# Kernel optimization log

Measured on AMD Instinct MI355X. Metric: run time of the kernel, lower is better.

Reference implementation:

```python
import jax, jax.numpy as jnp
import numpy as np

N_STACK = 32
ZERO_OFFSET = 1e-6
EPS = 1e-8
POW_EPS = 1e-12  # guard for 0**sharpen gradient


def _cos_sim(a, b):
    # a: [D] param, b: [B, D]; matches torch.cosine_similarity with eps=1e-8
    an = jnp.maximum(jnp.sqrt(jnp.sum(a * a)), EPS)
    bn = jnp.maximum(jnp.sqrt(jnp.sum(b * b, axis=-1)), EPS)
    return (b @ a) / (an * bn)


def _elu(x):
    return jnp.where(x > 0, x, jnp.expm1(x))


def setup_inputs() -> dict:
    key = jax.random.key(0)
    k0, k1, k2, k3 = jax.random.split(key, 4)
    B, T, D = 128, 256, 256
    return {
        "x": jax.random.normal(k0, (B, T, D), jnp.float32),
        "should_pop": jax.random.normal(k1, (D,), jnp.float32),
        "sharpen_pointer": jnp.array([5.0], jnp.float32),
        "latch_enable": jax.random.normal(k2, (D,), jnp.float32) * 0.01,
        "latch_init": jax.random.normal(k3, (B, D), jnp.float32),
    }


def _forward(x, should_pop, sharpen_pointer, latch_enable, latch_init):
    B, T, D = x.shape
    dtype = x.dtype
    stack0 = jnp.full((B, N_STACK, D), ZERO_OFFSET, dtype)
    ptr0 = jnp.full((B, N_STACK), ZERO_OFFSET, dtype).at[:, 0].set(1.0)
    sharpen = sharpen_pointer[0]

    def step(carry, inp):
        stack, ptr, latch = carry  # [B,N,D], [B,N], [B,D]
        # pop gate from PREVIOUS latch state (relay of length 1)
        pop = _elu(_cos_sim(should_pop, latch))            # [B]
        push = 1.0 - pop
        # push branch: advance pointer, write value at new slot
        p_push = jnp.roll(ptr, 1, axis=1)
        st_push = stack * (1.0 - p_push)[..., None] + inp[:, None, :] * p_push[..., None]
        # pop branch: erase current slot to zero_offset, retreat pointer
        st_pop = stack * (1.0 - ptr)[..., None] + ZERO_OFFSET * ptr[..., None]
        p_pop = jnp.roll(ptr, -1, axis=1)
        # superpose push/pop (null_op weight is exactly 0 in this module)
        new_stack = push[:, None, None] * st_push + pop[:, None, None] * st_pop
        new_ptr = push[:, None] * p_push + pop[:, None] * p_pop
        # sharpen pointer: relu, pow, renormalize
        p = jnp.maximum(jax.nn.relu(new_ptr), POW_EPS) ** sharpen
        p = p / jnp.maximum(jnp.sum(p, axis=1, keepdims=True), EPS)
        # read and gate output
        s = jnp.einsum('bnv,bn->bv', new_stack, p)
        out = pop[:, None] * s
        # latch update: gate = elu(cos(enable_param, inp)); dropout is eval-mode no-op
        g = _elu(_cos_sim(latch_enable, inp))
        new_latch = g[:, None] * inp + (1.0 - g)[:, None] * latch
        return (new_stack, p, new_latch), out

    _, outs = jax.lax.scan(step, (stack0, ptr0, latch_init), jnp.swapaxes(x, 0, 1))
    return jnp.swapaxes(outs, 0, 1)  # [B, T, D]


def reference(x, should_pop, sharpen_pointer, latch_enable, latch_init):
    return _forward(x, should_pop, sharpen_pointer, latch_enable, latch_init)
```

## Files before the change

kernel.cpp:

```cpp
#include <hip/hip_runtime.h>
#include <math.h>


#define NSTK 32
#define DDIM 256
#define ZO 1e-6f
#define EPSC 1e-8f
#define PEPS 1e-12f
#define TTILE 32
#define MAXT 1024
#define CH 4

__device__ __forceinline__ float elu_f(float c) {
    return (c > 0.f) ? c : expm1f(c);
}

__device__ __forceinline__ float dpp_xor1(float x) {
    return __int_as_float(__builtin_amdgcn_update_dpp(0, __float_as_int(x), 0xB1, 0xF, 0xF, true));
}
__device__ __forceinline__ float dpp_xor2(float x) {
    return __int_as_float(__builtin_amdgcn_update_dpp(0, __float_as_int(x), 0x4E, 0xF, 0xF, true));
}
__device__ __forceinline__ float dpp_halfmirror(float x) {
    return __int_as_float(__builtin_amdgcn_update_dpp(0, __float_as_int(x), 0x141, 0xF, 0xF, true));
}
__device__ __forceinline__ float dpp_mirror(float x) {
    return __int_as_float(__builtin_amdgcn_update_dpp(0, __float_as_int(x), 0x140, 0xF, 0xF, true));
}
__device__ __forceinline__ float swz_xor16(float x) {
    return __int_as_float(__builtin_amdgcn_ds_swizzle(__float_as_int(x), 0x401F));
}

__device__ __forceinline__ float xor16_sum(float x) {
    float a = x, b = x;
    asm("v_permlane16_swap_b32 %0, %1" : "+v"(a), "+v"(b));
    return a + b;
}
__device__ __forceinline__ float xor32_sum(float x) {
    float a = x, b = x;
    asm("v_permlane32_swap_b32 %0, %1" : "+v"(a), "+v"(b));
    return a + b;
}

__global__ void gate4_kernel(const float* __restrict__ vecs,
                             const float* __restrict__ par,
                             float* __restrict__ gout,
                             int T) {
    const int b = blockIdx.y;
    const int t = blockIdx.x * 4 + (threadIdx.x >> 6);
    const int lane = threadIdx.x & 63;
    const float4 v = *(const float4*)(vecs + ((size_t)b * T + t) * DDIM + lane * 4);
    const float4 p = *(const float4*)(par + lane * 4);
    float r0 = v.x * p.x + v.y * p.y + v.z * p.z + v.w * p.w;
    float r1 = v.x * v.x + v.y * v.y + v.z * v.z + v.w * v.w;
    float r2 = p.x * p.x + p.y * p.y + p.z * p.z + p.w * p.w;
#pragma unroll
    for (int off = 32; off >= 1; off >>= 1) {
        r0 += __shfl_xor(r0, off, 64);
        r1 += __shfl_xor(r1, off, 64);
        r2 += __shfl_xor(r2, off, 64);
    }
    if (lane == 0) {
        const float c = r0 / (fmaxf(sqrtf(r2), EPSC) * fmaxf(sqrtf(r1), EPSC));
        gout[(size_t)b * T + t] = elu_f(c);
    }
}

__global__ void latch_scan_kernel(const float* __restrict__ x,
                                  const float* __restrict__ latch0,
                                  const float* __restrict__ g,
                                  float* __restrict__ L,
                                  int T) {
    const int b = blockIdx.x >> 2;
    const int dt = blockIdx.x & 3;
    const int d = dt * 64 + threadIdx.x;
    const float* xb = x + (size_t)b * T * DDIM + d;
    const float* gb = g + (size_t)b * T;
    float* Lb = L + (size_t)b * T * DDIM + d;
    float l = latch0[(size_t)b * DDIM + d];
    for (int c = 0; c < T; c += 32) {
        float xv[32], gv[32];
#pragma unroll
        for (int i = 0; i < 32; i++) xv[i] = xb[(size_t)(c + i) * DDIM];
#pragma unroll
        for (int i = 0; i < 32; i++) gv[i] = gb[c + i];
#pragma unroll
        for (int i = 0; i < 32; i++) {
            Lb[(size_t)(c + i) * DDIM] = l;
            l = fmaf(gv[i], xv[i] - l, l);
        }
    }
}

__launch_bounds__(64, 1)
__global__ void ptr_scan_kernel(const float* __restrict__ pop_arr,
                                const float* __restrict__ sharpen_ptr,
                                float* __restrict__ Parr,
                                int T) {
    const int b0 = blockIdx.x * 2;
    const int tid = threadIdx.x;
    const int n = tid & 31;
    const int grp = tid >> 5;
    const float sharpen = sharpen_ptr[0];
    const bool sharp5 = (sharpen == 5.0f);

    __shared__ float pops[2 * MAXT];
    for (int i = tid; i < 2 * T; i += 64) pops[i] = pop_arr[(size_t)b0 * T + i];
    __syncthreads();
    const float* popg = pops + grp * T;
    float* Pb = Parr + (size_t)(b0 + grp) * T * 32;

    float u = (n == 0) ? 1.0f : ZO;
    float invu = 1.0f;
    int t = 0;

    auto step = [&](float pop) {
        const float push = 1.0f - pop;
        const float up = __shfl(u, (n + 31) & 31, 32);
        const float un = __shfl(u, (n + 1) & 31, 32);
        const float r = fmaf(push, up, pop * un);
        const float q = fmaxf(r * invu, PEPS);
        float unew;
        if (sharp5) { const float q2 = q * q, q4 = q2 * q2; unew = q4 * q; }
        else        { unew = exp2f(sharpen * log2f(q)); }
        float s = unew;
        s += dpp_xor1(s);
        s += dpp_xor2(s);
        s += dpp_halfmirror(s);
        s += dpp_mirror(s);
        s += swz_xor16(s);
        const float invn = 1.0f / fmaxf(s, EPSC);
        Pb[(size_t)t * 32 + n] = unew * invn;
        u = unew; invu = invn;
        t++;
    };

    const float4* p4 = (const float4*)popg;
    float4 cA0 = p4[0], cA1 = p4[1], cA2 = p4[2], cA3 = p4[3];
    for (int c = 0; c < T; c += 16) {
        float4 cB0, cB1, cB2, cB3;
        if (c + 16 < T) {
            const float4* pn4 = p4 + (c + 16) / 4;
            cB0 = pn4[0]; cB1 = pn4[1]; cB2 = pn4[2]; cB3 = pn4[3];
        }
        step(cA0.x); step(cA0.y); step(cA0.z); step(cA0.w);
        step(cA1.x); step(cA1.y); step(cA1.z); step(cA1.w);
        step(cA2.x); step(cA2.y); step(cA2.z); step(cA2.w);
        step(cA3.x); step(cA3.y); step(cA3.z); step(cA3.w);
        if (c + 16 < T) { cA0 = cB0; cA1 = cB1; cA2 = cB2; cA3 = cB3; }
    }
}

#define LOADC(PN, XN, PMN, POPN, t0) do {                                    \
    _Pragma("unroll") for (int i = 0; i < CH; i++) {                         \
        PN[i][0] = *(const float4*)(Pb + (size_t)((t0) + i) * 32);           \
        PN[i][1] = *(const float4*)(Pb + (size_t)((t0) + i) * 32 + 4);       \
        XN[i] = xb[(size_t)((t0) + i) * DDIM];                               \
        PMN[i] = Pm1b[(size_t)((t0) + i) * 32];                              \
        POPN[i] = popb[(t0) + i];                                            \
    } } while (0)

#define STEPS(PN, XN, PMN, POPN, tg) do {                                    \
    _Pragma("unroll") for (int i = 0; i < CH; i++) {                         \
        const float pop = POPN[i];                                           \
        const float push = 1.0f - pop;                                       \
        const float xv = XN[i];                                              \
        const float pn[8] = {PN[i][0].x, PN[i][0].y, PN[i][0].z, PN[i][0].w, \
                             PN[i][1].x, PN[i][1].y, PN[i][1].z, PN[i][1].w};\
        float acc = 0.f;                                                     \
        _Pragma("unroll") for (int j = 0; j < 8; j++) {                      \
            const float p_s = pc[j];                                         \
            const float pp_s = (j == 0) ? pm1 : pc[j - 1];                   \
            const float t0v = pop * p_s;                                     \
            const float m = fmaf(push, pp_s, t0v);                           \
            const float alpha = 1.0f - m;                                    \
            const float beta = push * pp_s;                                  \
            const float bxg = fmaf(beta, xv, ZO * t0v);                      \
            const float ns = fmaf(alpha, st[j], bxg);                        \
            st[j] = ns;                                                      \
            acc = fmaf(pn[j], ns, acc);                                      \
        }                                                                    \
        _Pragma("unroll") for (int j = 0; j < 8; j++) pc[j] = pn[j];         \
        pm1 = PMN[i];                                                        \
        acc = xor16_sum(acc);                                                \
        acc = xor32_sum(acc);                                                \
        if (lane < 16) ob[(size_t)((tg) + i) * DDIM] = pop * acc;            \
    } } while (0)

__launch_bounds__(64, 1)
__global__ void stack_kernel(const float* __restrict__ x,
                             const float* __restrict__ Parr,
                             const float* __restrict__ pop_arr,
                             float* __restrict__ out,
                             int T) {
    const int b = blockIdx.y;
    const int dtile = blockIdx.x;
    const int lane = threadIdx.x;
    const int dsub = lane & 15;
    const int ng = lane >> 4;

    const float* Pb = Parr + (size_t)b * T * 32 + ng * 8;
    const int pm1_idx = (ng * 8 + 31) & 31;
    const float* Pm1b = Parr + (size_t)b * T * 32 + pm1_idx;
    const float* xb = x + (size_t)b * T * DDIM + dtile * 16 + dsub;
    const float* popb = pop_arr + (size_t)b * T;
    float* ob = out + (size_t)b * T * DDIM + dtile * 16 + dsub;

    float st[8], pc[8];
#pragma unroll
    for (int j = 0; j < 8; j++) { st[j] = ZO; pc[j] = ZO; }
    if (ng == 0) pc[0] = 1.0f;
    float pm1 = ZO;

    float4 PA[CH][2], PB[CH][2];
    float xA[CH], xB[CH], pmA[CH], pmB[CH], popA[CH], popB[CH];

    LOADC(PA, xA, pmA, popA, 0);
    for (int c = 0; c < T; c += 2 * CH) {
        if (c + CH < T) LOADC(PB, xB, pmB, popB, c + CH);
        STEPS(PA, xA, pmA, popA, c);
        if (c + 2 * CH < T) LOADC(PA, xA, pmA, popA, c + 2 * CH);
        STEPS(PB, xB, pmB, popB, c + CH);
    }
}

__launch_bounds__(256, 1)
__global__ void neuralstack_kernel(const float* __restrict__ x,
                                   const float* __restrict__ should_pop,
                                   const float* __restrict__ sharpen_ptr,
                                   const float* __restrict__ latch_enable,
                                   const float* __restrict__ latch_init,
                                   float* __restrict__ out,
                                   int T) {
    const int b = blockIdx.x;
    const int tid = threadIdx.x;
    const int wave = tid >> 6;
    const int lane = tid & 63;
    __shared__ float red[2][16];
    const float sp_d = should_pop[tid];
    const float le_d = latch_enable[tid];
    const float sharpen = sharpen_ptr[0];
    float latch = latch_init[(size_t)b * DDIM + tid];
    float a0 = sp_d * sp_d, a1 = le_d * le_d;
#pragma unroll
    for (int off = 32; off >= 1; off >>= 1) {
        a0 += __shfl_xor(a0, off, 64);
        a1 += __shfl_xor(a1, off, 64);
    }
    if (lane == 0) { red[0][wave * 4] = a0; red[0][wave * 4 + 1] = a1; }
    __syncthreads();
    const float an_sp = fmaxf(sqrtf(red[0][0] + red[0][4] + red[0][8] + red[0][12]), EPSC);
    const float an_le = fmaxf(sqrtf(red[0][1] + red[0][5] + red[0][9] + red[0][13]), EPSC);
    __syncthreads();
    float st[NSTK], ptr[NSTK];
#pragma unroll
    for (int n = 0; n < NSTK; n++) { st[n] = ZO; ptr[n] = (n == 0) ? 1.0f : ZO; }
    const float* xb = x + (size_t)b * T * DDIM + tid;
    float* ob = out + (size_t)b * T * DDIM + tid;
    const bool sharp5 = (sharpen == 5.0f);
    float inp = xb[0];
    for (int t = 0; t < T; t++) {
        const int tn = (t + 1 < T) ? (t + 1) : (T - 1);
        const float inp_next = xb[(size_t)tn * DDIM];
        float r0 = sp_d * latch, r1 = latch * latch, r2 = le_d * inp, r3 = inp * inp;
#pragma unroll
        for (int off = 32; off >= 1; off >>= 1) {
            r0 += __shfl_xor(r0, off, 64);
            r1 += __shfl_xor(r1, off, 64);
            r2 += __shfl_xor(r2, off, 64);
            r3 += __shfl_xor(r3, off, 64);
        }
        const int buf = t & 1;
        if (lane == 0) {
            red[buf][wave * 4] = r0; red[buf][wave * 4 + 1] = r1;
            red[buf][wave * 4 + 2] = r2; red[buf][wave * 4 + 3] = r3;
        }
        __syncthreads();
        const float s0 = red[buf][0] + red[buf][4] + red[buf][8] + red[buf][12];
        const float s1 = red[buf][1] + red[buf][5] + red[buf][9] + red[buf][13];
        const float s2 = red[buf][2] + red[buf][6] + red[buf][10] + red[buf][14];
        const float s3 = red[buf][3] + red[buf][7] + red[buf][11] + red[buf][15];
        const float pop = elu_f(s0 / (an_sp * fmaxf(sqrtf(s1), EPSC)));
        const float push = 1.0f - pop;
        const float g = elu_f(s2 / (an_le * fmaxf(sqrtf(s3), EPSC)));
        float q[NSTK];
#pragma unroll
        for (int n = 0; n < NSTK; n++) {
            const float pp = ptr[(n + NSTK - 1) & (NSTK - 1)];
            const float pn = ptr[(n + 1) & (NSTK - 1)];
            q[n] = fmaxf(push * pp + pop * pn, PEPS);
        }
        if (sharp5) {
#pragma unroll
            for (int n = 0; n < NSTK; n++) { const float v = q[n], v2 = v * v; q[n] = v2 * v2 * v; }
        } else {
#pragma unroll
            for (int n = 0; n < NSTK; n++) q[n] = exp2f(sharpen * log2f(q[n]));
        }
        float qa = 0.f, qb = 0.f, qc = 0.f, qd = 0.f;
#pragma unroll
        for (int n = 0; n < NSTK; n += 4) { qa += q[n]; qb += q[n+1]; qc += q[n+2]; qd += q[n+3]; }
        const float inv = 1.0f / fmaxf((qa + qb) + (qc + qd), EPSC);
        float sacc = 0.f;
#pragma unroll
        for (int n = 0; n < NSTK; n++) {
            const float pp = ptr[(n + NSTK - 1) & (NSTK - 1)];
            const float pc_ = ptr[n];
            const float ns = push * (st[n] + pp * (inp - st[n])) + pop * (st[n] + pc_ * (ZO - st[n]));
            st[n] = ns;
            sacc += ns * (q[n] * inv);
        }
#pragma unroll
        for (int n = 0; n < NSTK; n++) ptr[n] = q[n] * inv;
        ob[(size_t)t * DDIM] = pop * sacc;
        latch = fmaf(g, inp - latch, latch);
        inp = inp_next;
    }
}

extern "C" void kernel_launch(void* const* d_in, const int* in_sizes, int n_in,
                              void* d_out, int out_size, void* d_ws, size_t ws_size,
                              hipStream_t stream) {
    const float* x = (const float*)d_in[0];
    const float* should_pop = (const float*)d_in[1];
    const float* sharpen_ptr = (const float*)d_in[2];
    const float* latch_enable = (const float*)d_in[3];
    const float* latch_init = (const float*)d_in[4];
    float* out = (float*)d_out;

    const int D = in_sizes[1];
    const int B = in_sizes[4] / D;
    const int T = in_sizes[0] / in_sizes[4];
    (void)n_in; (void)out_size;

    const size_t BT = (size_t)B * T;
    const size_t off_g = 0;
    const size_t off_pop = BT;
    const size_t off_L = 2 * BT;
    const size_t off_P = off_L + BT * D;
    const size_t need_floats = off_P + BT * 32;

    if (ws_size < need_floats * sizeof(float) || D != DDIM ||
        (T % TTILE) != 0 || (B % 2) != 0 || T > MAXT) {
        neuralstack_kernel<<<B, 256, 0, stream>>>(x, should_pop, sharpen_ptr,
                                                  latch_enable, latch_init, out, T);
        return;
    }

    float* ws = (float*)d_ws;
    float* g = ws + off_g;
    float* pop = ws + off_pop;
    float* L = ws + off_L;
    float* P = ws + off_P;

    gate4_kernel<<<dim3(T / 4, B), 256, 0, stream>>>(x, latch_enable, g, T);
    latch_scan_kernel<<<B * 4, 64, 0, stream>>>(x, latch_init, g, L, T);
    gate4_kernel<<<dim3(T / 4, B), 256, 0, stream>>>(L, should_pop, pop, T);
    ptr_scan_kernel<<<B / 2, 64, 0, stream>>>(pop, sharpen_ptr, P, T);
    stack_kernel<<<dim3(D / 16, B), 64, 0, stream>>>(x, P, pop, out, T);
}
```

Baseline: 237.2 us.

## Precompute per-step stack coefficients in a separate kernel before the stack scan

Adds a coef_kernel that computes, for every batch, step and stack slot, the alpha/beta/zero-offset/read-weight coefficients from the pointer and pop arrays. It stores them as float4 in the workspace region that previously held the latch buffer. The stack scan then only does two FMAs plus the accumulate per slot, and no longer tracks the previous pointer in registers. The trade is an extra kernel launch and about 4x more coefficient traffic per step, read redundantly by all 16 d-tiles. The prefetch depth also drops from 4-step chunks to a single step ahead.

```diff
diff --git a/kernel.cpp b/kernel.cpp
--- a/kernel.cpp
+++ b/kernel.cpp
@@ -7,9 +7,7 @@
 #define ZO 1e-6f
 #define EPSC 1e-8f
 #define PEPS 1e-12f
-#define TTILE 32
 #define MAXT 1024
-#define CH 4
 
 __device__ __forceinline__ float elu_f(float c) {
     return (c > 0.f) ? c : expm1f(c);
@@ -151,45 +149,60 @@
     }
 }
 
-#define LOADC(PN, XN, PMN, POPN, t0) do {                                    \
-    _Pragma("unroll") for (int i = 0; i < CH; i++) {                         \
-        PN[i][0] = *(const float4*)(Pb + (size_t)((t0) + i) * 32);           \
-        PN[i][1] = *(const float4*)(Pb + (size_t)((t0) + i) * 32 + 4);       \
-        XN[i] = xb[(size_t)((t0) + i) * DDIM];                               \
-        PMN[i] = Pm1b[(size_t)((t0) + i) * 32];                              \
-        POPN[i] = popb[(t0) + i];                                            \
-    } } while (0)
-
-#define STEPS(PN, XN, PMN, POPN, tg) do {                                    \
-    _Pragma("unroll") for (int i = 0; i < CH; i++) {                         \
-        const float pop = POPN[i];                                           \
-        const float push = 1.0f - pop;                                       \
-        const float xv = XN[i];                                              \
-        const float pn[8] = {PN[i][0].x, PN[i][0].y, PN[i][0].z, PN[i][0].w, \
-                             PN[i][1].x, PN[i][1].y, PN[i][1].z, PN[i][1].w};\
-        float acc = 0.f;                                                     \
-        _Pragma("unroll") for (int j = 0; j < 8; j++) {                      \
-            const float p_s = pc[j];                                         \
-            const float pp_s = (j == 0) ? pm1 : pc[j - 1];                   \
-            const float t0v = pop * p_s;                                     \
-            const float m = fmaf(push, pp_s, t0v);                           \
-            const float alpha = 1.0f - m;                                    \
-            const float beta = push * pp_s;                                  \
-            const float bxg = fmaf(beta, xv, ZO * t0v);                      \
-            const float ns = fmaf(alpha, st[j], bxg);                        \
-            st[j] = ns;                                                      \
-            acc = fmaf(pn[j], ns, acc);                                      \
-        }                                                                    \
-        _Pragma("unroll") for (int j = 0; j < 8; j++) pc[j] = pn[j];         \
-        pm1 = PMN[i];                                                        \
-        acc = xor16_sum(acc);                                                \
-        acc = xor32_sum(acc);                                                \
-        if (lane < 16) ob[(size_t)((tg) + i) * DDIM] = pop * acc;            \
-    } } while (0)
+__global__ void coef_kernel(const float* __restrict__ Parr,
+                            const float* __restrict__ pop_arr,
+                            float* __restrict__ Carr,
+                            int T) {
+    const int b = blockIdx.y;
+    const int tid = threadIdx.x;
+    const int t = blockIdx.x * 2 + (tid >> 5);
+    const int n = tid & 31;
+    const float* Pb = Parr + (size_t)b * T * 32;
+    const float pop = pop_arr[(size_t)b * T + t];
+    const float push = 1.0f - pop;
+    float p, pp;
+    if (t == 0) {
+        p  = (n == 0) ? 1.0f : ZO;
+        pp = (n == 1) ? 1.0f : ZO;
+    } else {
+        p  = Pb[(size_t)(t - 1) * 32 + n];
+        pp = Pb[(size_t)(t - 1) * 32 + ((n + 31) & 31)];
+    }
+    const float w = Pb[(size_t)t * 32 + n];
+    const float t0v = pop * p;
+    const float m = fmaf(push, pp, t0v);
+    const float alpha = 1.0f - m;
+    const float beta = push * pp;
+    const float g2 = ZO * t0v;
+    float4 cv;
+    cv.x = alpha; cv.y = beta; cv.z = g2; cv.w = w;
+    ((float4*)Carr)[(size_t)b * T * 32 + (size_t)t * 32 + n] = cv;
+}
+
+#define SLOAD(CN, XV, POPV, tt) do {                                         \
+    _Pragma("unroll") for (int k = 0; k < 8; k++)                            \
+        CN[k] = Cb[(size_t)(tt) * 32 + k];                                   \
+    XV = xb[(size_t)(tt) * DDIM];                                            \
+    POPV = popb[(tt)];                                                       \
+} while (0)
+
+#define SSTEP(CN, XV, POPV, tt) do {                                         \
+    float acc = 0.f;                                                         \
+    _Pragma("unroll") for (int j = 0; j < 8; j++) {                          \
+        const float4 c = CN[j];                                              \
+        const float bxg = fmaf(c.y, XV, c.z);                                \
+        const float ns = fmaf(c.x, st[j], bxg);                              \
+        st[j] = ns;                                                          \
+        acc = fmaf(c.w, ns, acc);                                            \
+    }                                                                        \
+    acc = xor16_sum(acc);                                                    \
+    acc = xor32_sum(acc);                                                    \
+    if (lane < 16) ob[(size_t)(tt) * DDIM] = POPV * acc;                     \
+} while (0)
 
 __launch_bounds__(64, 1)
 __global__ void stack_kernel(const float* __restrict__ x,
-                             const float* __restrict__ Parr,
+                             const float* __restrict__ Carr,
                              const float* __restrict__ pop_arr,
                              float* __restrict__ out,
                              int T) {
@@ -199,28 +212,24 @@
     const int dsub = lane & 15;
     const int ng = lane >> 4;
 
-    const float* Pb = Parr + (size_t)b * T * 32 + ng * 8;
-    const int pm1_idx = (ng * 8 + 31) & 31;
-    const float* Pm1b = Parr + (size_t)b * T * 32 + pm1_idx;
+    const float4* Cb = (const float4*)Carr + (size_t)b * T * 32 + ng * 8;
     const float* xb = x + (size_t)b * T * DDIM + dtile * 16 + dsub;
     const float* popb = pop_arr + (size_t)b * T;
     float* ob = out + (size_t)b * T * DDIM + dtile * 16 + dsub;
 
-    float st[8], pc[8];
-#pragma unroll
-    for (int j = 0; j < 8; j++) { st[j] = ZO; pc[j] = ZO; }
-    if (ng == 0) pc[0] = 1.0f;
-    float pm1 = ZO;
-
-    float4 PA[CH][2], PB[CH][2];
-    float xA[CH], xB[CH], pmA[CH], pmB[CH], popA[CH], popB[CH];
-
-    LOADC(PA, xA, pmA, popA, 0);
-    for (int c = 0; c < T; c += 2 * CH) {
-        if (c + CH < T) LOADC(PB, xB, pmB, popB, c + CH);
-        STEPS(PA, xA, pmA, popA, c);
-        if (c + 2 * CH < T) LOADC(PA, xA, pmA, popA, c + 2 * CH);
-        STEPS(PB, xB, pmB, popB, c + CH);
+    float st[8];
+#pragma unroll
+    for (int j = 0; j < 8; j++) st[j] = ZO;
+
+    float4 CA[8], CB[8];
+    float xA, xB, popA, popB;
+
+    SLOAD(CA, xA, popA, 0);
+    for (int t = 0; t < T; t += 2) {
+        SLOAD(CB, xB, popB, t + 1);
+        SSTEP(CA, xA, popA, t);
+        if (t + 2 < T) SLOAD(CA, xA, popA, t + 2);
+        SSTEP(CB, xB, popB, t + 1);
     }
 }
 
@@ -341,7 +350,7 @@
     const size_t need_floats = off_P + BT * 32;
 
     if (ws_size < need_floats * sizeof(float) || D != DDIM ||
-        (T % TTILE) != 0 || (B % 2) != 0 || T > MAXT) {
+        (T % 16) != 0 || (B % 2) != 0 || T > MAXT) {
         neuralstack_kernel<<<B, 256, 0, stream>>>(x, should_pop, sharpen_ptr,
                                                   latch_enable, latch_init, out, T);
         return;
@@ -351,11 +360,13 @@
     float* g = ws + off_g;
     float* pop = ws + off_pop;
     float* L = ws + off_L;
+    float* C = ws + off_L;
     float* P = ws + off_P;
 
     gate4_kernel<<<dim3(T / 4, B), 256, 0, stream>>>(x, latch_enable, g, T);
     latch_scan_kernel<<<B * 4, 64, 0, stream>>>(x, latch_init, g, L, T);
     gate4_kernel<<<dim3(T / 4, B), 256, 0, stream>>>(L, should_pop, pop, T);
     ptr_scan_kernel<<<B / 2, 64, 0, stream>>>(pop, sharpen_ptr, P, T);
-    stack_kernel<<<dim3(D / 16, B), 64, 0, stream>>>(x, P, pop, out, T);
-}
+    coef_kernel<<<dim3(T / 2, B), 64, 0, stream>>>(P, pop, C, T);
+    stack_kernel<<<dim3(D / 16, B), 64, 0, stream>>>(x, C, pop, out, T);
+}
```

Result: slower. 272.1 us (+14.7%).
